# Kernel optimization log

Hardware: AMD Instinct MI355X
Metric: run time of the kernel (lower is better)

Reference implementation:

```python
import jax, jax.numpy as jnp
import numpy as np

MASK_VALUE = -1000000.0


def setup_inputs() -> dict:
    key = jax.random.key(0)
    k1, k2, k3, k4 = jax.random.split(key, 4)
    B, Lq, Lk, d = 32, 1024, 1024, 128
    return {
        "query": jax.random.normal(k1, (B, Lq, d), dtype=jnp.float32),
        "key": jax.random.normal(k2, (B, Lk, d), dtype=jnp.float32),
        "value": jax.random.normal(k3, (B, Lk, d), dtype=jnp.float32),
        "valid_length": jax.random.randint(k4, (B,), 0, Lk, dtype=jnp.int64),
    }


def reference(query, key, value, valid_length):
    # query [B, Lq, d], key/value [B, Lk, d], valid_length [B]
    d = query.shape[-1]
    # scores [B, Lq, Lk]
    scores = jnp.einsum("bqd,bkd->bqk", query, key) / jnp.sqrt(jnp.float32(d))
    Lk = key.shape[1]
    # mask positions >= valid_length with -1e6 (per-batch, broadcast over Lq)
    pos = jnp.arange(Lk)  # [Lk]
    mask = pos[None, None, :] >= valid_length[:, None, None]  # [B, 1, Lk]
    scores = jnp.where(mask, MASK_VALUE, scores)
    attn = jax.nn.softmax(scores, axis=-1)
    # dropout p=0.0 in eval -> identity
    return jnp.einsum("bqk,bkd->bqd", attn, value)
```

## Files before the change

kernel.cpp:

```cpp
#include <hip/hip_runtime.h>

#define B_N 32
#define LQ  1024
#define LK  1024
#define DH  128

typedef __attribute__((ext_vector_type(4))) float f32x4;
typedef __attribute__((ext_vector_type(8))) short s16x8;

__device__ inline unsigned short f2bf(float f) {
    union { float f; unsigned u; } c; c.f = f;
    unsigned u = c.u;
    u += 0x7fffu + ((u >> 16) & 1u);
    return (unsigned short)(u >> 16);
}

#define ESCALE 0.12751743f

__global__ __launch_bounds__(256)
void prep_kv(const float* __restrict__ K, const float* __restrict__ V,
             unsigned short* __restrict__ Kb, unsigned short* __restrict__ Vt)
{
    __shared__ float vlds[32 * 132];
    const int tid  = threadIdx.x;
    const int lane = tid & 63;
    const int wv   = tid >> 6;
    const int n    = lane & 15;
    const int quad = lane >> 4;
    union { s16x8 v; unsigned short u[8]; } t;

    if (blockIdx.x < 2048) {
        const int w = blockIdx.x * 4 + wv;
        const int b = w >> 8, rem = w & 255, tt = rem >> 2, s = rem & 3;
        const float* p = K + ((size_t)b * LK + tt * 16 + n) * DH + s * 32 + quad * 8;
        const float4 a = *(const float4*)p;
        const float4 c = *(const float4*)(p + 4);
        t.u[0] = f2bf(a.x); t.u[1] = f2bf(a.y); t.u[2] = f2bf(a.z); t.u[3] = f2bf(a.w);
        t.u[4] = f2bf(c.x); t.u[5] = f2bf(c.y); t.u[6] = f2bf(c.z); t.u[7] = f2bf(c.w);
        *(s16x8*)(Kb + (size_t)w * 512 + lane * 8) = t.v;
    } else {
        const int vt = blockIdx.x - 2048;
        const int b  = vt >> 5, kt = vt & 31;
        const float4* src = (const float4*)(V + ((size_t)b * LK + kt * 32) * DH);
        #pragma unroll
        for (int h = 0; h < 4; ++h) {
            const int idx = h * 256 + tid;
            const int row = idx >> 5, c4 = idx & 31;
            *(float4*)&vlds[row * 132 + c4 * 4] = src[idx];
        }
        __syncthreads();
        #pragma unroll
        for (int h = 0; h < 2; ++h) {
            const int c8 = wv * 2 + h;
            #pragma unroll
            for (int j = 0; j < 8; ++j)
                t.u[j] = f2bf(vlds[(quad * 8 + j) * 132 + c8 * 16 + n]);
            const int v = b * 256 + kt * 8 + c8;
            *(s16x8*)(Vt + (size_t)v * 512 + lane * 8) = t.v;
        }
    }
}

#define PSTRIDE 72

__global__ __launch_bounds__(64, 2)
void attn_fwd(const float* __restrict__ Q, const unsigned short* __restrict__ Kb,
              const unsigned short* __restrict__ Vt, const int* __restrict__ VL,
              float* __restrict__ O)
{
    __shared__ unsigned short Plds[16 * PSTRIDE];

    const int lane = threadIdx.x & 63;
    const int quad = lane >> 4;
    const int m16  = lane & 15;

    const int b  = blockIdx.x & 31;
    const int qt = blockIdx.x >> 5;
    const int q0 = qt * 16;

    const int vl = VL[b];
    const int nch = (vl > 0) ? ((vl + 63) >> 6) : 16;
    const float emaskval = (vl == 0) ? 1.0f : 0.0f;

    s16x8 qf[4];
    {
        const float* qrow = Q + ((size_t)b * LQ + q0 + m16) * DH + quad * 8;
        #pragma unroll
        for (int s = 0; s < 4; ++s) {
            const float4 a = *(const float4*)(qrow + s * 32);
            const float4 c = *(const float4*)(qrow + s * 32 + 4);
            union { s16x8 v; unsigned short u[8]; } t;
            t.u[0] = f2bf(a.x); t.u[1] = f2bf(a.y); t.u[2] = f2bf(a.z); t.u[3] = f2bf(a.w);
            t.u[4] = f2bf(c.x); t.u[5] = f2bf(c.y); t.u[6] = f2bf(c.z); t.u[7] = f2bf(c.w);
            qf[s] = t.v;
        }
    }

    f32x4 o[8];
    #pragma unroll
    for (int c8 = 0; c8 < 8; ++c8) o[c8] = (f32x4){0.f, 0.f, 0.f, 0.f};
    float lrun[4] = {0.f, 0.f, 0.f, 0.f};

    const unsigned short* kbase = Kb + (size_t)b * (256 * 512) + lane * 8;
    const unsigned short* vbase = Vt + (size_t)b * (256 * 512) + lane * 8;

    for (int kb = 0; kb < nch; ++kb) {
        f32x4 st[4];
        #pragma unroll
        for (int tn = 0; tn < 4; ++tn) st[tn] = (f32x4){0.f, 0.f, 0.f, 0.f};
        const unsigned short* kc = kbase + (size_t)kb * (16 * 512);
        #pragma unroll
        for (int tn = 0; tn < 4; ++tn) {
            #pragma unroll
            for (int s = 0; s < 4; ++s) {
                const s16x8 kf = *(const s16x8*)(kc + (tn * 4 + s) * 512);
                st[tn] = __builtin_amdgcn_mfma_f32_16x16x32_bf16(qf[s], kf, st[tn], 0, 0, 0);
            }
        }

        const unsigned short* vc = vbase + (size_t)kb * (16 * 512);
        s16x8 vfA[8];
        #pragma unroll
        for (int i = 0; i < 8; ++i) vfA[i] = *(const s16x8*)(vc + i * 512);

        const bool maskc = (kb * 64 + 64 > vl);
        #pragma unroll
        for (int r = 0; r < 4; ++r) {
            float e[4];
            #pragma unroll
            for (int tn = 0; tn < 4; ++tn) {
                e[tn] = __builtin_amdgcn_exp2f(st[tn][r] * ESCALE);
                if (maskc && (kb * 64 + tn * 16 + m16 >= vl)) e[tn] = emaskval;
            }
            lrun[r] += (e[0] + e[1]) + (e[2] + e[3]);
            const int prow = (quad * 4 + r) * PSTRIDE;
            #pragma unroll
            for (int tn = 0; tn < 4; ++tn) Plds[prow + tn * 16 + m16] = f2bf(e[tn]);
        }

        __asm__ volatile("s_waitcnt lgkmcnt(0)" ::: "memory");
        const s16x8 pf0 = *(const s16x8*)&Plds[m16 * PSTRIDE + quad * 8];
        const s16x8 pf1 = *(const s16x8*)&Plds[m16 * PSTRIDE + 32 + quad * 8];

        #pragma unroll
        for (int c8 = 0; c8 < 8; ++c8)
            o[c8] = __builtin_amdgcn_mfma_f32_16x16x32_bf16(pf0, vfA[c8], o[c8], 0, 0, 0);
        s16x8 vfB[8];
        #pragma unroll
        for (int i = 0; i < 8; ++i) vfB[i] = *(const s16x8*)(vc + (8 + i) * 512);
        #pragma unroll
        for (int c8 = 0; c8 < 8; ++c8)
            o[c8] = __builtin_amdgcn_mfma_f32_16x16x32_bf16(pf1, vfB[c8], o[c8], 0, 0, 0);
    }

    const size_t obase = ((size_t)b * LQ + q0 + quad * 4) * DH + m16;
    #pragma unroll
    for (int r = 0; r < 4; ++r) {
        float L = lrun[r];
        L += __shfl_xor(L, 1);
        L += __shfl_xor(L, 2);
        L += __shfl_xor(L, 4);
        L += __shfl_xor(L, 8);
        const float inv = 1.0f / L;
        #pragma unroll
        for (int c8 = 0; c8 < 8; ++c8)
            O[obase + (size_t)r * DH + c8 * 16] = o[c8][r] * inv;
    }
}

extern "C" void kernel_launch(void* const* d_in, const int* in_sizes, int n_in,
                              void* d_out, int out_size, void* d_ws, size_t ws_size,
                              hipStream_t stream) {
    const float* Q  = (const float*)d_in[0];
    const float* K  = (const float*)d_in[1];
    const float* V  = (const float*)d_in[2];
    const int*   VL = (const int*)d_in[3];
    float* O = (float*)d_out;
    (void)in_sizes; (void)n_in; (void)out_size; (void)ws_size;

    unsigned short* Kb = (unsigned short*)d_ws;
    unsigned short* Vt = Kb + (size_t)B_N * 256 * 512;

    prep_kv<<<dim3(3072), dim3(256), 0, stream>>>(K, V, Kb, Vt);
    attn_fwd<<<dim3(B_N * (LQ / 16)), dim3(64), 0, stream>>>(Q, Kb, Vt, VL, O);
}
```

Measured before the change: 131.4 us.

## Register-prefetch next K/V chunk in attention loop and stage K prep through LDS

The attention kernel now loads the K and V fragments for the next 64-key chunk into registers while the current chunk's MFMAs and softmax run, so global-load latency overlaps with compute. Launch bounds drop the two-waves-per-SIMD minimum so the extra 32 vector registers fit. The prep kernel now converts K through an LDS tile with coalesced loads, as V already was, which cuts its grid from 3072 to 2048 blocks. The cost is much higher register pressure in attn_fwd, which may lower occupancy.

```diff
diff --git a/kernel.cpp b/kernel.cpp
--- a/kernel.cpp
+++ b/kernel.cpp
@@ -21,49 +21,56 @@
 void prep_kv(const float* __restrict__ K, const float* __restrict__ V,
              unsigned short* __restrict__ Kb, unsigned short* __restrict__ Vt)
 {
-    __shared__ float vlds[32 * 132];
+    __shared__ float tl[32 * 132];
     const int tid  = threadIdx.x;
     const int lane = tid & 63;
     const int wv   = tid >> 6;
     const int n    = lane & 15;
     const int quad = lane >> 4;
-    union { s16x8 v; unsigned short u[8]; } t;
-
-    if (blockIdx.x < 2048) {
-        const int w = blockIdx.x * 4 + wv;
-        const int b = w >> 8, rem = w & 255, tt = rem >> 2, s = rem & 3;
-        const float* p = K + ((size_t)b * LK + tt * 16 + n) * DH + s * 32 + quad * 8;
-        const float4 a = *(const float4*)p;
-        const float4 c = *(const float4*)(p + 4);
-        t.u[0] = f2bf(a.x); t.u[1] = f2bf(a.y); t.u[2] = f2bf(a.z); t.u[3] = f2bf(a.w);
-        t.u[4] = f2bf(c.x); t.u[5] = f2bf(c.y); t.u[6] = f2bf(c.z); t.u[7] = f2bf(c.w);
-        *(s16x8*)(Kb + (size_t)w * 512 + lane * 8) = t.v;
+
+    const bool isK = blockIdx.x < 1024;
+    const int  t   = isK ? blockIdx.x : (blockIdx.x - 1024);
+    const int  b   = t >> 5, kt = t & 31;
+
+    const float4* src = (const float4*)((isK ? K : V) + ((size_t)b * LK + kt * 32) * DH);
+    #pragma unroll
+    for (int h = 0; h < 4; ++h) {
+        const int idx = h * 256 + tid;
+        const int row = idx >> 5, c4 = idx & 31;
+        *(float4*)&tl[row * 132 + c4 * 4] = src[idx];
+    }
+    __syncthreads();
+
+    union { s16x8 v; unsigned short u[8]; } t8;
+    if (isK) {
+        #pragma unroll
+        for (int h = 0; h < 2; ++h) {
+            const int f = wv * 2 + h;
+            const int tt2 = f >> 2, s = f & 3;
+            const float* p = &tl[(tt2 * 16 + n) * 132 + s * 32 + quad * 8];
+            const float4 a = *(const float4*)p;
+            const float4 c = *(const float4*)(p + 4);
+            t8.u[0] = f2bf(a.x); t8.u[1] = f2bf(a.y); t8.u[2] = f2bf(a.z); t8.u[3] = f2bf(a.w);
+            t8.u[4] = f2bf(c.x); t8.u[5] = f2bf(c.y); t8.u[6] = f2bf(c.z); t8.u[7] = f2bf(c.w);
+            const int w = b * 256 + (kt * 2 + tt2) * 4 + s;
+            *(s16x8*)(Kb + (size_t)w * 512 + lane * 8) = t8.v;
+        }
     } else {
-        const int vt = blockIdx.x - 2048;
-        const int b  = vt >> 5, kt = vt & 31;
-        const float4* src = (const float4*)(V + ((size_t)b * LK + kt * 32) * DH);
-        #pragma unroll
-        for (int h = 0; h < 4; ++h) {
-            const int idx = h * 256 + tid;
-            const int row = idx >> 5, c4 = idx & 31;
-            *(float4*)&vlds[row * 132 + c4 * 4] = src[idx];
-        }
-        __syncthreads();
         #pragma unroll
         for (int h = 0; h < 2; ++h) {
             const int c8 = wv * 2 + h;
             #pragma unroll
             for (int j = 0; j < 8; ++j)
-                t.u[j] = f2bf(vlds[(quad * 8 + j) * 132 + c8 * 16 + n]);
+                t8.u[j] = f2bf(tl[(quad * 8 + j) * 132 + c8 * 16 + n]);
             const int v = b * 256 + kt * 8 + c8;
-            *(s16x8*)(Vt + (size_t)v * 512 + lane * 8) = t.v;
+            *(s16x8*)(Vt + (size_t)v * 512 + lane * 8) = t8.v;
         }
     }
 }
 
 #define PSTRIDE 72
 
-__global__ __launch_bounds__(64, 2)
+__global__ __launch_bounds__(64)
 void attn_fwd(const float* __restrict__ Q, const unsigned short* __restrict__ Kb,
               const unsigned short* __restrict__ Vt, const int* __restrict__ VL,
               float* __restrict__ O)
@@ -104,24 +111,29 @@
     const unsigned short* kbase = Kb + (size_t)b * (256 * 512) + lane * 8;
     const unsigned short* vbase = Vt + (size_t)b * (256 * 512) + lane * 8;
 
+    s16x8 kf[16], vfA[8], vfB[8];
+    #pragma unroll
+    for (int i = 0; i < 16; ++i) kf[i] = *(const s16x8*)(kbase + i * 512);
+    #pragma unroll
+    for (int i = 0; i < 8; ++i) vfA[i] = *(const s16x8*)(vbase + i * 512);
+    #pragma unroll
+    for (int i = 0; i < 8; ++i) vfB[i] = *(const s16x8*)(vbase + (8 + i) * 512);
+
     for (int kb = 0; kb < nch; ++kb) {
         f32x4 st[4];
         #pragma unroll
         for (int tn = 0; tn < 4; ++tn) st[tn] = (f32x4){0.f, 0.f, 0.f, 0.f};
-        const unsigned short* kc = kbase + (size_t)kb * (16 * 512);
         #pragma unroll
         for (int tn = 0; tn < 4; ++tn) {
             #pragma unroll
-            for (int s = 0; s < 4; ++s) {
-                const s16x8 kf = *(const s16x8*)(kc + (tn * 4 + s) * 512);
-                st[tn] = __builtin_amdgcn_mfma_f32_16x16x32_bf16(qf[s], kf, st[tn], 0, 0, 0);
-            }
-        }
-
-        const unsigned short* vc = vbase + (size_t)kb * (16 * 512);
-        s16x8 vfA[8];
-        #pragma unroll
-        for (int i = 0; i < 8; ++i) vfA[i] = *(const s16x8*)(vc + i * 512);
+            for (int s = 0; s < 4; ++s)
+                st[tn] = __builtin_amdgcn_mfma_f32_16x16x32_bf16(qf[s], kf[tn * 4 + s], st[tn], 0, 0, 0);
+        }
+
+        const int knx = (kb + 1 < nch) ? (kb + 1) : kb;
+        const unsigned short* kcn = kbase + (size_t)knx * (16 * 512);
+        #pragma unroll
+        for (int i = 0; i < 16; ++i) kf[i] = *(const s16x8*)(kcn + i * 512);
 
         const bool maskc = (kb * 64 + 64 > vl);
         #pragma unroll
@@ -142,15 +154,18 @@
         const s16x8 pf0 = *(const s16x8*)&Plds[m16 * PSTRIDE + quad * 8];
         const s16x8 pf1 = *(const s16x8*)&Plds[m16 * PSTRIDE + 32 + quad * 8];
 
+        const unsigned short* vcn = vbase + (size_t)knx * (16 * 512);
+
         #pragma unroll
         for (int c8 = 0; c8 < 8; ++c8)
             o[c8] = __builtin_amdgcn_mfma_f32_16x16x32_bf16(pf0, vfA[c8], o[c8], 0, 0, 0);
-        s16x8 vfB[8];
-        #pragma unroll
-        for (int i = 0; i < 8; ++i) vfB[i] = *(const s16x8*)(vc + (8 + i) * 512);
+        #pragma unroll
+        for (int i = 0; i < 8; ++i) vfA[i] = *(const s16x8*)(vcn + i * 512);
         #pragma unroll
         for (int c8 = 0; c8 < 8; ++c8)
             o[c8] = __builtin_amdgcn_mfma_f32_16x16x32_bf16(pf1, vfB[c8], o[c8], 0, 0, 0);
+        #pragma unroll
+        for (int i = 0; i < 8; ++i) vfB[i] = *(const s16x8*)(vcn + (8 + i) * 512);
     }
 
     const size_t obase = ((size_t)b * LQ + q0 + quad * 4) * DH + m16;
@@ -181,6 +196,6 @@
     unsigned short* Kb = (unsigned short*)d_ws;
     unsigned short* Vt = Kb + (size_t)B_N * 256 * 512;
 
-    prep_kv<<<dim3(3072), dim3(256), 0, stream>>>(K, V, Kb, Vt);
+    prep_kv<<<dim3(2048), dim3(256), 0, stream>>>(K, V, Kb, Vt);
     attn_fwd<<<dim3(B_N * (LQ / 16)), dim3(64), 0, stream>>>(Q, Kb, Vt, VL, O);
 }
```

Result: no change. 129.0 us (-1.8%).
